# Optimization experiments

Hardware: AMD Instinct MI355X
Metric: run time of the kernel (lower is better)

The kernel has to match this reference:

```python
import jax, jax.numpy as jnp
import numpy as np
from jax import lax

B, T_IN, E, T_OUT, N_MEL = 64, 512, 512, 800, 80
P, A_LSTM, D_LSTM, ATT, NF, K = 256, 1024, 1024, 128, 32, 31
PAD = (K - 1) // 2


def setup_inputs() -> dict:
    key = jax.random.key(0)
    ks = jax.random.split(key, 24)
    s = 0.02
    d = {}
    d['encoder_outputs'] = jax.random.normal(ks[0], (B, T_IN, E), jnp.float32)
    d['decoder_inputs'] = jax.random.normal(ks[1], (B, N_MEL, T_OUT), jnp.float32)
    d['text_lengths'] = jax.random.randint(ks[2], (B,), T_IN // 2, T_IN + 1)
    # prenet (two bias-free linears)
    d['Wp1'] = jax.random.normal(ks[3], (N_MEL, P), jnp.float32) * s
    d['Wp2'] = jax.random.normal(ks[4], (P, P), jnp.float32) * s
    # attention LSTMCell: input = prenet_dim + encoder_lstm_dim
    d['Wi_a'] = jax.random.normal(ks[5], (P + E, 4 * A_LSTM), jnp.float32) * s
    d['Wh_a'] = jax.random.normal(ks[6], (A_LSTM, 4 * A_LSTM), jnp.float32) * s
    d['b_a'] = jnp.zeros((4 * A_LSTM,), jnp.float32)
    # location-sensitive attention
    d['Wq'] = jax.random.normal(ks[7], (A_LSTM, ATT), jnp.float32) * s
    d['Wm'] = jax.random.normal(ks[8], (E, ATT), jnp.float32) * s
    d['Wv'] = jax.random.normal(ks[9], (ATT,), jnp.float32) * s
    d['Kloc'] = jax.random.normal(ks[10], (NF, 2, K), jnp.float32) * s   # OIH conv kernel
    d['Wloc'] = jax.random.normal(ks[11], (NF, ATT), jnp.float32) * s
    # decoder LSTMCell: input = attention_lstm_dim + encoder_lstm_dim
    d['Wi_d'] = jax.random.normal(ks[12], (A_LSTM + E, 4 * D_LSTM), jnp.float32) * s
    d['Wh_d'] = jax.random.normal(ks[13], (D_LSTM, 4 * D_LSTM), jnp.float32) * s
    d['b_d'] = jnp.zeros((4 * D_LSTM,), jnp.float32)
    # projections from [decoder_hidden ; attention_context]
    d['Wproj'] = jax.random.normal(ks[14], (D_LSTM + E, N_MEL), jnp.float32) * s
    d['bproj'] = jnp.zeros((N_MEL,), jnp.float32)
    d['Wgate'] = jax.random.normal(ks[15], (D_LSTM + E,), jnp.float32) * s
    d['bgate'] = jnp.zeros((), jnp.float32)
    return d


def _lstm_cell(x, h, c, Wi, Wh, b):
    g = x @ Wi + h @ Wh + b
    i, f, gg, o = jnp.split(g, 4, axis=-1)  # torch LSTMCell gate order i,f,g,o
    c = jax.nn.sigmoid(f) * c + jax.nn.sigmoid(i) * jnp.tanh(gg)
    h = jax.nn.sigmoid(o) * jnp.tanh(c)
    return h, c


def reference(encoder_outputs, decoder_inputs, text_lengths,
              Wp1, Wp2, Wi_a, Wh_a, b_a, Wq, Wm, Wv, Kloc, Wloc,
              Wi_d, Wh_d, b_d, Wproj, bproj, Wgate, bgate):
    b, t_in, e = encoder_outputs.shape
    t_out = decoder_inputs.shape[2]
    valid = jnp.arange(t_in)[None, :] < text_lengths[:, None]  # [B,T_in]
    pm = encoder_outputs @ Wm                                   # processed memory [B,T_in,ATT]

    # parse_decoder_inputs + go frame -> [T_out, B, n_mel] (n_frames_per_step=1)
    x = jnp.transpose(decoder_inputs, (2, 0, 1))
    x = jnp.concatenate([jnp.zeros((1, b, N_MEL), x.dtype), x], 0)[:t_out]
    # prenet over all steps (dropout disabled: eval-mode reference)
    h = jax.nn.relu(jax.nn.relu(x @ Wp1) @ Wp2)                 # [T_out,B,P]

    def step(carry, xt):
        ah, ac, dh, dc, aw, awc, ctx = carry
        ah, ac = _lstm_cell(jnp.concatenate([xt, ctx], -1), ah, ac, Wi_a, Wh_a, b_a)
        cat = jnp.stack([aw, awc], axis=1)                      # [B,2,T_in]
        loc = lax.conv_general_dilated(cat, Kloc, (1,), [(PAD, PAD)],
                                       dimension_numbers=('NCH', 'OIH', 'NCH'))  # [B,NF,T_in]
        ploc = jnp.einsum('bft,fa->bta', loc, Wloc)             # [B,T_in,ATT]
        energies = jnp.einsum('bta,a->bt',
                              jnp.tanh((ah @ Wq)[:, None, :] + ploc + pm), Wv)
        energies = jnp.where(valid, energies, -1e9)
        aw = jax.nn.softmax(energies, axis=1)                   # [B,T_in]
        ctx = jnp.einsum('bt,bte->be', aw, encoder_outputs)
        awc = awc + aw
        dh, dc = _lstm_cell(jnp.concatenate([ah, ctx], -1), dh, dc, Wi_d, Wh_d, b_d)
        hc = jnp.concatenate([dh, ctx], -1)
        mel = hc @ Wproj + bproj                                # [B,N_MEL]
        gate = hc @ Wgate + bgate                               # [B]
        return (ah, ac, dh, dc, aw, awc, ctx), (mel, gate, aw)

    z = lambda *s: jnp.zeros(s, encoder_outputs.dtype)
    init = (z(b, A_LSTM), z(b, A_LSTM), z(b, D_LSTM), z(b, D_LSTM),
            z(b, t_in), z(b, t_in), z(b, e))
    _, (mels, gates, aws) = lax.scan(step, init, h)
    mel_outputs = jnp.transpose(mels, (1, 2, 0))                # [B,N_MEL,T_out]
    gate_outputs = jnp.transpose(gates, (1, 0))                 # [B,T_out]
    alignments = jnp.transpose(aws, (1, 0, 2))                  # [B,T_out,T_in]
    return mel_outputs, gate_outputs, alignments
```

## Files before the change

kernel.cpp:

```cpp
#include <hip/hip_runtime.h>
#include <math.h>

#define NBLK 256
#define NTHR 512

#define BB    64
#define TIN   512
#define EEE   512
#define TOUTT 800
#define NMEL  80
#define PPP   256
#define ALS   1024
#define DLS   1024
#define ATTD  128
#define KA    1792
#define KD    2560

typedef _Float16 f16;
typedef f16 f16x8 __attribute__((ext_vector_type(8)));
typedef f16 f16x2 __attribute__((ext_vector_type(2)));
typedef float f32x4 __attribute__((ext_vector_type(4)));
typedef unsigned long long u64;

#define WTA_OFF   0ull
#define WTD_OFF   3670016ull
#define PM16_OFF  8912896ull
#define ENC16_OFF 11010048ull
#define PRE_OFF   19398656ull
#define XA_OFF    25952256ull
#define XD_OFF    26066944ull
#define AH16_OFF  26230784ull
#define DH16_OFF  26263552ull
#define CTX16_OFF 26296320ull
#define EN_OFF    26329088ull
#define WQT_OFF   26361856ull
#define WPJT_OFF  26427392ull
#define WP1T_OFF  26489600ull
#define WP2T_OFF  26499840ull
#define WLP_OFF   26532608ull
#define KLP_OFF   26534656ull
#define BAR_OFF   26535648ull

#define PL_O   0
#define RED_O  512
#define QL_O   528
#define PART_O 664

__device__ __forceinline__ float sigm(float x) { return 1.0f / (1.0f + __expf(-x)); }
__device__ __forceinline__ float ftanh(float x) {
  return 1.f - 2.f / (__expf(2.f * x) + 1.f);
}

union pk32 { unsigned u; f16x2 h; float f; };
__device__ __forceinline__ unsigned packh2(float a, float b) {
  pk32 p; p.h[0] = (f16)a; p.h[1] = (f16)b; return p.u;
}

__device__ __forceinline__ u64 ld64cg(const void* p) {
  return __hip_atomic_load((const u64*)p, __ATOMIC_RELAXED, __HIP_MEMORY_SCOPE_AGENT);
}
__device__ __forceinline__ void stu16cg(void* p, unsigned short v) {
  __hip_atomic_store((unsigned short*)p, v, __ATOMIC_RELAXED, __HIP_MEMORY_SCOPE_AGENT);
}
__device__ __forceinline__ void stu32cg(void* p, unsigned v) {
  __hip_atomic_store((unsigned*)p, v, __ATOMIC_RELAXED, __HIP_MEMORY_SCOPE_AGENT);
}
__device__ __forceinline__ f16x8 ld128cg(const f16* p) {
  union { u64 q[2]; f16x8 v; } r;
  r.q[0] = ld64cg(p);
  r.q[1] = ld64cg(p + 4);
  return r.v;
}

__device__ __forceinline__ size_t fragaddr(int b, int k) {
  return (size_t)(k >> 5) * 2048 + (size_t)(b >> 4) * 512 +
         (size_t)(((b & 15) + (((k & 31) >> 3) << 4)) << 3) + (k & 7);
}

__device__ __forceinline__ void gbar(unsigned* bar, unsigned& n, bool full) {
  n += 1;
  __syncthreads();
  if (threadIdx.x == 0) {
    if (full) __threadfence();
    __hip_atomic_fetch_add(&bar[(blockIdx.x & 15) << 4], 1u, __ATOMIC_RELAXED, __HIP_MEMORY_SCOPE_AGENT);
  }
  if (threadIdx.x < 64) {
    const unsigned tgt = n * 16u;
    const unsigned g = (threadIdx.x & 15) << 4;
    asm volatile("" ::: "memory");
    while (!__all((threadIdx.x >= 16) ||
                  (__hip_atomic_load(&bar[g], __ATOMIC_RELAXED, __HIP_MEMORY_SCOPE_AGENT) >= tgt)))
      __builtin_amdgcn_s_sleep(1);
    asm volatile("" ::: "memory");
    if (full) __threadfence();
  }
  __syncthreads();
}

__global__ void __launch_bounds__(256) transA(const float* __restrict__ Wi,
                                              const float* __restrict__ Wh,
                                              f16* __restrict__ Wt) {
  __shared__ float tile[64][65];
  const int tid = threadIdx.x;
  const int kb = (int)blockIdx.x % 28;
  const int cb = (int)blockIdx.x / 28;
  const int k0 = kb * 64, c0 = cb * 64;
  for (int i = tid; i < 4096; i += 256) {
    const int r = i >> 6, c = i & 63;
    const int k = k0 + r;
    const float v = (k < 768) ? Wi[(size_t)k * 4096 + c0 + c]
                              : Wh[(size_t)(k - 768) * 4096 + c0 + c];
    tile[c][r] = v;
  }
  __syncthreads();
  for (int i = tid; i < 4096; i += 256) {
    const int c = i >> 6, kk = i & 63;
    Wt[(size_t)(c0 + c) * KA + k0 + kk] = (f16)tile[c][kk];
  }
}

__global__ void __launch_bounds__(256) transD(const float* __restrict__ Wi,
                                              const float* __restrict__ Wh,
                                              f16* __restrict__ Wt) {
  __shared__ float tile[64][65];
  const int tid = threadIdx.x;
  const int kb = (int)blockIdx.x % 40;
  const int cb = (int)blockIdx.x / 40;
  const int k0 = kb * 64, c0 = cb * 64;
  for (int i = tid; i < 4096; i += 256) {
    const int r = i >> 6, c = i & 63;
    const int k = k0 + r;
    const float v = (k < 1536) ? Wi[(size_t)k * 4096 + c0 + c]
                               : Wh[(size_t)(k - 1536) * 4096 + c0 + c];
    tile[c][r] = v;
  }
  __syncthreads();
  for (int i = tid; i < 4096; i += 256) {
    const int c = i >> 6, kk = i & 63;
    Wt[(size_t)(c0 + c) * KD + k0 + kk] = (f16)tile[c][kk];
  }
}

__global__ void __launch_bounds__(128) pmk(const float* __restrict__ enc,
                                           const float* __restrict__ Wm,
                                           f16* __restrict__ pm16) {
  __shared__ float er[512];
  const int tid = threadIdx.x;
  const int b = (int)blockIdx.x >> 9, tt = (int)blockIdx.x & 511;
  for (int i = tid; i < 512; i += 128) er[i] = enc[((size_t)b * TIN + tt) * EEE + i];
  __syncthreads();
  float s = 0.f;
  #pragma unroll 4
  for (int k = 0; k < 512; ++k) s += er[k] * Wm[k * ATTD + tid];
  pm16[((size_t)b * TIN + tt) * ATTD + tid] = (f16)s;
}

__global__ void __launch_bounds__(512) enc16k(const float* __restrict__ enc,
                                              f16* __restrict__ e16) {
  const size_t i = ((size_t)blockIdx.x * 512 + threadIdx.x) * 8;
  const float4 v0 = *reinterpret_cast<const float4*>(enc + i);
  const float4 v1 = *reinterpret_cast<const float4*>(enc + i + 4);
  f16x8 o;
  o[0] = (f16)v0.x; o[1] = (f16)v0.y; o[2] = (f16)v0.z; o[3] = (f16)v0.w;
  o[4] = (f16)v1.x; o[5] = (f16)v1.y; o[6] = (f16)v1.z; o[7] = (f16)v1.w;
  *reinterpret_cast<f16x8*>(e16 + i) = o;
}

__global__ void __launch_bounds__(256) kwk(const float* __restrict__ Kloc,
                                           const float* __restrict__ Wloc,
                                           f16* __restrict__ kwb) {
  const int idx = (int)blockIdx.x * 256 + (int)threadIdx.x;
  const int kc = idx >> 7, a = idx & 127;
  const int k = kc >> 1, cch = kc & 1;
  float s = 0.f;
  if (k < 31) {
    #pragma unroll 8
    for (int f = 0; f < 32; ++f)
      s += Kloc[f * 62 + cch * 31 + k] * Wloc[f * 128 + a];
  }
  const int ct = a >> 4, n = a & 15;
  const int ks = kc >> 5, kcl = kc & 31, kch = kcl >> 3, j = kcl & 7;
  kwb[((size_t)(ct * 2 + ks) * 64 + (kch * 16 + n)) * 8 + j] = (f16)s;
}

__global__ void __launch_bounds__(512) transAux(const float* __restrict__ Wq,
                                                const float* __restrict__ Wproj,
                                                const float* __restrict__ Wgate,
                                                const float* __restrict__ Wp1,
                                                const float* __restrict__ Wp2,
                                                f16* __restrict__ wqt,
                                                f16* __restrict__ wpjt,
                                                f16* __restrict__ wp1t,
                                                f16* __restrict__ wp2t) {
  const int idx = (int)blockIdx.x * 512 + (int)threadIdx.x;
  if (idx < 131072) {
    const int a = idx >> 10, k = idx & 1023;
    wqt[idx] = (f16)Wq[k * 128 + a];
  } else if (idx < 131072 + 124416) {
    const int j = idx - 131072;
    const int m = j / 1536, k = j % 1536;
    wpjt[j] = (f16)(m < 80 ? Wproj[k * 80 + m] : Wgate[k]);
  } else if (idx < 131072 + 124416 + 20480) {
    const int j = idx - (131072 + 124416);
    const int col = j / 80, k = j % 80;
    wp1t[j] = (f16)Wp1[k * 256 + col];
  } else if (idx < 131072 + 124416 + 20480 + 65536) {
    const int j = idx - (131072 + 124416 + 20480);
    const int col = j >> 8, k = j & 255;
    wp2t[j] = (f16)Wp2[k * 256 + col];
  }
}

__global__ void __launch_bounds__(512) prenetk(const float* __restrict__ dec_in,
                                               const f16* __restrict__ wp1t,
                                               const f16* __restrict__ wp2t,
                                               f16* __restrict__ pre) {
  __shared__ float xl[64 * 80];
  __shared__ f16 h1l[64 * 264];
  const int t = (int)blockIdx.x;
  const int tid = threadIdx.x;
  f16* out = pre + (size_t)t * 16384;
  if (t == 0) {
    unsigned* o32 = (unsigned*)out;
    for (int i = tid; i < 8192; i += 512) o32[i] = 0u;
    return;
  }
  for (int i = tid; i < 5120; i += 512) {
    const int b = i / 80, m = i % 80;
    xl[b * 80 + m] = dec_in[(size_t)b * (NMEL * TOUTT) + (size_t)m * TOUTT + (t - 1)];
  }
  __syncthreads();
  {
    const int col = tid & 255, bh = tid >> 8;
    for (int bb = 0; bb < 32; ++bb) {
      const int b = bh * 32 + bb;
      float s = 0.f;
      #pragma unroll 4
      for (int k = 0; k < 80; ++k) s += xl[b * 80 + k] * (float)wp1t[col * 80 + k];
      h1l[b * 264 + col] = (f16)fmaxf(s, 0.f);
    }
  }
  __syncthreads();
  {
    const int col = tid & 255, bh = tid >> 8;
    for (int bb = 0; bb < 32; ++bb) {
      const int b = bh * 32 + bb;
      float s = 0.f;
      #pragma unroll 4
      for (int k = 0; k < 256; ++k) s += (float)h1l[b * 264 + k] * (float)wp2t[col * 256 + k];
      out[fragaddr(b, col)] = (f16)fmaxf(s, 0.f);
    }
  }
}

__device__ __forceinline__ void lstm_tail(int bid, int tid, float* smemf,
                                          const f32x4 c, int kh, int mt, int lane,
                                          const float* __restrict__ bias, float& creg,
                                          f16* __restrict__ h16,
                                          f16* frag1, int k1off,
                                          f16* frag2, int k2off) {
  float* Call = smemf;
  float* CallB = smemf + 1024;
  const int r0 = mt * 16 + (lane >> 4) * 4;
  const int n = lane & 15;
  if (kh == 1) {
    #pragma unroll
    for (int j = 0; j < 4; ++j) CallB[(r0 + j) * 16 + n] = c[j];
  }
  __syncthreads();
  if (kh == 0) {
    #pragma unroll
    for (int j = 0; j < 4; ++j) Call[(r0 + j) * 16 + n] = c[j] + CallB[(r0 + j) * 16 + n];
  }
  __syncthreads();
  if (tid < 256) {
    const int b = tid & 63, q = tid >> 6;
    const int cc = bid * 4 + q;
    const float g0 = Call[b * 16 + q]      + bias[cc];
    const float g1 = Call[b * 16 + 4 + q]  + bias[1024 + cc];
    const float g2 = Call[b * 16 + 8 + q]  + bias[2048 + cc];
    const float g3 = Call[b * 16 + 12 + q] + bias[3072 + cc];
    const float cn = sigm(g1) * creg + sigm(g0) * ftanh(g2);
    creg = cn;
    const float h = sigm(g3) * ftanh(cn);
    pk32 hp; hp.h[0] = (f16)h; hp.h[1] = (f16)0.f;
    const unsigned short hu = (unsigned short)(hp.u & 0xFFFFu);
    stu16cg(h16 + (size_t)b * 1024 + cc, hu);
    if (frag1) stu16cg(frag1 + fragaddr(b, k1off + cc), hu);
    if (frag2) stu16cg(frag2 + fragaddr(b, k2off + cc), hu);
  }
}

__device__ __forceinline__ void do_melgate(int b, int half, int tcol,
                                           const f16* __restrict__ dh16,
                                           const f16* __restrict__ ctx16p,
                                           const f16* __restrict__ wpjt,
                                           const float* __restrict__ bproj,
                                           const float* __restrict__ bgate,
                                           float* __restrict__ out_mel,
                                           float* __restrict__ out_gate,
                                           float* smem) {
  const int tid = threadIdx.x;
  __syncthreads();
  u64* dhl = (u64*)smem;
  u64* ctl = (u64*)smem + 256;
  if (tid < 256)      dhl[tid] = ld64cg((const u64*)(dh16 + (size_t)b * 1024) + tid);
  else if (tid < 384) ctl[tid - 256] = ld64cg((const u64*)(ctx16p + (size_t)b * 512) + (tid - 256));
  __syncthreads();
  float* melp = smem + 768;
  const int nrow = half ? 40 : 41;
  const int ml = tid / 12, kq = tid % 12;
  if (ml < nrow) {
    const int m = half * 41 + ml;
    const f16* wr = wpjt + (size_t)m * 1536 + kq * 128;
    const f16* xl = (kq < 8) ? ((const f16*)dhl + kq * 128)
                             : ((const f16*)ctl + (kq - 8) * 128);
    float s = 0.f;
    #pragma unroll
    for (int c8 = 0; c8 < 16; ++c8) {
      const f16x8 xv = *reinterpret_cast<const f16x8*>(xl + c8 * 8);
      const f16x8 wv = *reinterpret_cast<const f16x8*>(wr + c8 * 8);
      #pragma unroll
      for (int j = 0; j < 8; ++j) s += (float)xv[j] * (float)wv[j];
    }
    melp[ml * 12 + kq] = s;
  }
  __syncthreads();
  if (tid < nrow) {
    float s = 0.f;
    #pragma unroll
    for (int j = 0; j < 12; ++j) s += melp[tid * 12 + j];
    const int m = half * 41 + tid;
    if (m < 80) out_mel[(size_t)b * NMEL * TOUTT + (size_t)m * TOUTT + tcol] = s + bproj[m];
    else        out_gate[(size_t)b * TOUTT + tcol] = s + bgate[0];
  }
}

__global__ void __launch_bounds__(NTHR, 1)
decoder_loop(const int* __restrict__ tlen,
             const float* __restrict__ b_a, const float* __restrict__ b_d,
             const float* __restrict__ Wv,
             const float* __restrict__ bproj, const float* __restrict__ bgate,
             const f16* __restrict__ wta_h, const f16* __restrict__ wtd_h,
             const f16* __restrict__ pm16, const f16* __restrict__ enc16,
             const f16* __restrict__ pre_h,
             const f16* __restrict__ wqt, const f16* __restrict__ wpjt,
             const f16* __restrict__ kwb,
             f16* __restrict__ xa_h, f16* __restrict__ xd_h,
             f16* __restrict__ ah16, f16* __restrict__ dh16,
             f16* __restrict__ ctx16,
             unsigned* bar,
             float* __restrict__ out_mel, float* __restrict__ out_gate,
             float* __restrict__ out_align) {
  __shared__ f16 wfA[28672];
  __shared__ f16 wfD[40960];
  __shared__ float smem[2048];
  __shared__ unsigned awb[544];

  const int tid = threadIdx.x;
  const int bid = (int)blockIdx.x;
  const int lane = tid & 63;
  const int w = tid >> 6;
  const int mt = w & 3, kh = w >> 2;
  const int b = bid & 63;
  const int chn = bid >> 6;
  unsigned syncn = 0;

  for (int i = tid; i < 3584; i += NTHR) {
    const int ks = i >> 6, l = i & 63;
    const int n = l & 15, kc = (l >> 4) * 8;
    const int gcol = (n >> 2) * 1024 + bid * 4 + (n & 3);
    const uint4 v = *reinterpret_cast<const uint4*>(wta_h + (size_t)gcol * KA + ks * 32 + kc);
    *reinterpret_cast<uint4*>(&wfA[(size_t)i * 8]) = v;
  }
  for (int i = tid; i < 5120; i += NTHR) {
    const int ks = i >> 6, l = i & 63;
    const int n = l & 15, kc = (l >> 4) * 8;
    const int gcol = (n >> 2) * 1024 + bid * 4 + (n & 3);
    const uint4 v = *reinterpret_cast<const uint4*>(wtd_h + (size_t)gcol * KD + ks * 32 + kc);
    *reinterpret_cast<uint4*>(&wfD[(size_t)i * 8]) = v;
  }
  for (int i = tid; i < 544; i += NTHR) awb[i] = 0u;
  {
    unsigned* za = (unsigned*)xa_h;
    const int gid = bid * NTHR + tid;
    for (int i = gid; i < 278528; i += NBLK * NTHR) za[i] = 0u;
  }
  gbar(bar, syncn, true);

  const int len = tlen[b];
  float awcf = 0.f;
  float cregA = 0.f, cregD = 0.f;

  for (int t = 0; t <= TOUTT; ++t) {
    if (t > 0) {
      const f16* xdP = xd_h + (size_t)((t - 1) & 1) * 163840;
      const f16* abase = xdP + (size_t)(kh * 40) * 2048 + mt * 512 + lane * 8;
      const f16* bbase = wfD + ((size_t)(kh * 40) * 64 + lane) * 8;
      f32x4 c = {0.f, 0.f, 0.f, 0.f};
      #pragma unroll 8
      for (int ks = 0; ks < 40; ++ks) {
        const f16x8 af = ld128cg(abase + (size_t)ks * 2048);
        const f16x8 bf = *reinterpret_cast<const f16x8*>(bbase + (size_t)ks * 512);
        c = __builtin_amdgcn_mfma_f32_16x16x32_f16(af, bf, c, 0, 0, 0);
      }
      lstm_tail(bid, tid, smem, c, kh, mt, lane, b_d, cregD, dh16,
                xd_h + (size_t)(t & 1) * 163840, 1536, (f16*)0, 0);
    }
    if (t < TOUTT) {
      const f16* xaP = xa_h + (size_t)(t & 1) * 114688;
      const f16* preP = pre_h + (size_t)t * 16384;
      const f16* bbase = wfA + ((size_t)(kh * 28) * 64 + lane) * 8;
      f32x4 c = {0.f, 0.f, 0.f, 0.f};
      #pragma unroll 8
      for (int ks = 0; ks < 28; ++ks) {
        const int kg = kh * 28 + ks;
        const f16* ap = (kg < 8) ? preP : xaP;
        const f16x8 af = (kg < 8)
            ? *reinterpret_cast<const f16x8*>(ap + (size_t)kg * 2048 + mt * 512 + lane * 8)
            : ld128cg(ap + (size_t)kg * 2048 + mt * 512 + lane * 8);
        const f16x8 bf = *reinterpret_cast<const f16x8*>(bbase + (size_t)ks * 512);
        c = __builtin_amdgcn_mfma_f32_16x16x32_f16(af, bf, c, 0, 0, 0);
      }
      lstm_tail(bid, tid, smem, c, kh, mt, lane, b_a, cregA, ah16,
                xa_h + (size_t)((t + 1) & 1) * 114688, 768,
                xd_h + (size_t)(t & 1) * 163840, 0);
    }
    gbar(bar, syncn, false);

    if (t == TOUTT) {
      if (chn == 1 || chn == 2)
        do_melgate(b, chn - 1, TOUTT - 1, dh16, ctx16 + (size_t)((TOUTT - 1) & 1) * 32768,
                   wpjt, bproj, bgate, out_mel, out_gate, smem);
      break;
    }

    {
      u64* ahl = (u64*)smem;
      if (tid < 256) ahl[tid] = ld64cg((const u64*)(ah16 + (size_t)b * 1024) + tid);
      __syncthreads();
      {
        const int a = tid & 127, kq = tid >> 7;
        const f16* arow = (const f16*)ahl + kq * 256;
        const f16* wr = wqt + (size_t)a * 1024 + kq * 256;
        float s = 0.f;
        #pragma unroll 8
        for (int c8 = 0; c8 < 32; ++c8) {
          const f16x8 xv = *reinterpret_cast<const f16x8*>(arow + c8 * 8);
          const f16x8 wv = *reinterpret_cast<const f16x8*>(wr + c8 * 8);
          #pragma unroll
          for (int j = 0; j < 8; ++j) s += (float)xv[j] * (float)wv[j];
        }
        smem[PART_O + kq * 128 + a] = s;
      }
      __syncthreads();
      if (tid < 128) {
        const int a = tid;
        smem[QL_O + a + (a >> 5)] = smem[PART_O + a] + smem[PART_O + 128 + a] +
                                    smem[PART_O + 256 + a] + smem[PART_O + 384 + a];
      }
      __syncthreads();

      float qlv[8], wvv[8];
      #pragma unroll
      for (int ct = 0; ct < 8; ++ct) {
        const int a = ct * 16 + (lane & 15);
        qlv[ct] = smem[QL_O + a + (a >> 5)];
        wvv[ct] = Wv[a];
      }

      for (int rt4 = 0; rt4 < 4; ++rt4) {
        const int rt = w * 4 + rt4;
        const int r_a = rt * 16 + (lane & 15);
        f32x4 c[8];
        #pragma unroll
        for (int ct = 0; ct < 8; ++ct) c[ct] = (f32x4){0.f, 0.f, 0.f, 0.f};
        #pragma unroll
        for (int ks = 0; ks < 2; ++ks) {
          const int tap = (lane >> 4) * 4 + ks * 16;
          union { unsigned u[4]; f16x8 v; } af;
          #pragma unroll
          for (int q4 = 0; q4 < 4; ++q4) af.u[q4] = awb[1 + r_a + tap + q4];
          #pragma unroll
          for (int ct = 0; ct < 8; ++ct) {
            const f16x8 bf = *reinterpret_cast<const f16x8*>(
                kwb + ((size_t)(ct * 2 + ks) * 64 + lane) * 8);
            c[ct] = __builtin_amdgcn_mfma_f32_16x16x32_f16(af.v, bf, c[ct], 0, 0, 0);
          }
        }
        float ep[4] = {0.f, 0.f, 0.f, 0.f};
        #pragma unroll
        for (int ct = 0; ct < 8; ++ct) {
          const int a = ct * 16 + (lane & 15);
          #pragma unroll
          for (int j = 0; j < 4; ++j) {
            const int r = rt * 16 + ((lane >> 4) << 2) + j;
            const float pmv = (float)pm16[(size_t)(b * TIN + r) * ATTD + a];
            ep[j] += wvv[ct] * ftanh(qlv[ct] + c[ct][j] + pmv);
          }
        }
        #pragma unroll
        for (int j = 0; j < 4; ++j) {
          ep[j] += __shfl_xor(ep[j], 1);
          ep[j] += __shfl_xor(ep[j], 2);
          ep[j] += __shfl_xor(ep[j], 4);
          ep[j] += __shfl_xor(ep[j], 8);
        }
        if ((lane & 15) == 0) {
          #pragma unroll
          for (int j = 0; j < 4; ++j)
            smem[PL_O + rt * 16 + ((lane >> 4) << 2) + j] = ep[j];
        }
      }

      const float ee = (tid < len) ? smem[PL_O + tid] : -1e30f;
      float m = ee;
      #pragma unroll
      for (int o = 32; o > 0; o >>= 1) m = fmaxf(m, __shfl_xor(m, o));
      if (lane == 0) smem[RED_O + w] = m;
      __syncthreads();
      if (tid == 0) {
        float mm = smem[RED_O];
        #pragma unroll
        for (int i = 1; i < 8; ++i) mm = fmaxf(mm, smem[RED_O + i]);
        smem[RED_O + 8] = mm;
      }
      __syncthreads();
      const float M = smem[RED_O + 8];
      const float p = (tid < len) ? __expf(ee - M) : 0.f;
      float s = p;
      #pragma unroll
      for (int o = 32; o > 0; o >>= 1) s += __shfl_xor(s, o);
      if (lane == 0) smem[RED_O + w] = s;
      __syncthreads();
      if (tid == 0) {
        float ss = smem[RED_O];
        #pragma unroll
        for (int i = 1; i < 8; ++i) ss += smem[RED_O + i];
        smem[RED_O + 8] = ss;
      }
      __syncthreads();
      const float an = p * (1.f / smem[RED_O + 8]);
      smem[PL_O + tid] = an;
      awcf += an;
      awb[16 + tid] = packh2(an, awcf);
      if (chn == 0) out_align[((size_t)b * TOUTT + t) * TIN + tid] = an;
      __syncthreads();

      {
        const int eo = lane & 15, sub4 = lane >> 4;
        float a8[8];
        #pragma unroll
        for (int i = 0; i < 8; ++i) a8[i] = 0.f;
        const f16* ebase = enc16 + (size_t)(b * TIN) * EEE + chn * 128 + eo * 8;
        #pragma unroll 4
        for (int j = 0; j < 16; ++j) {
          const int tj = w * 64 + sub4 * 16 + j;
          const float wv = smem[PL_O + tj];
          const f16x8 ev = __builtin_nontemporal_load(
              reinterpret_cast<const f16x8*>(ebase + (size_t)tj * EEE));
          #pragma unroll
          for (int i = 0; i < 8; ++i) a8[i] += wv * (float)ev[i];
        }
        #pragma unroll
        for (int i = 0; i < 8; ++i) {
          a8[i] += __shfl_xor(a8[i], 16);
          a8[i] += __shfl_xor(a8[i], 32);
        }
        if (lane < 16) {
          #pragma unroll
          for (int i = 0; i < 8; ++i) smem[PART_O + w * 128 + eo * 8 + i] = a8[i];
        }
      }
      __syncthreads();
      if (tid < 128) {
        float v = 0.f;
        #pragma unroll
        for (int ww = 0; ww < 8; ++ww) v += smem[PART_O + ww * 128 + tid];
        smem[PL_O + tid] = v;
      }
      __syncthreads();
      if (tid < 64) {
        const int ecol = chn * 128 + 2 * tid;
        const unsigned pv = packh2(smem[PL_O + 2 * tid], smem[PL_O + 2 * tid + 1]);
        stu32cg((unsigned*)(xa_h + (size_t)((t + 1) & 1) * 114688 + fragaddr(b, 256 + ecol)), pv);
        stu32cg((unsigned*)(xd_h + (size_t)(t & 1) * 163840 + fragaddr(b, 1024 + ecol)), pv);
        stu32cg((unsigned*)(ctx16 + (size_t)(t & 1) * 32768 + (size_t)b * 512 + ecol), pv);
      }
      if (t > 0 && (chn == 1 || chn == 2))
        do_melgate(b, chn - 1, t - 1, dh16, ctx16 + (size_t)((t - 1) & 1) * 32768,
                   wpjt, bproj, bgate, out_mel, out_gate, smem);
    }
    gbar(bar, syncn, false);
  }
}

extern "C" void kernel_launch(void* const* d_in, const int* in_sizes, int n_in,
                              void* d_out, int out_size, void* d_ws, size_t ws_size,
                              hipStream_t stream) {
  (void)in_sizes; (void)n_in; (void)out_size; (void)ws_size;
  const float* enc    = (const float*)d_in[0];
  const float* dec_in = (const float*)d_in[1];
  const int*   tlen   = (const int*)d_in[2];
  const float* Wp1    = (const float*)d_in[3];
  const float* Wp2    = (const float*)d_in[4];
  const float* Wi_a   = (const float*)d_in[5];
  const float* Wh_a   = (const float*)d_in[6];
  const float* b_a    = (const float*)d_in[7];
  const float* Wq     = (const float*)d_in[8];
  const float* Wm     = (const float*)d_in[9];
  const float* Wv     = (const float*)d_in[10];
  const float* Kloc   = (const float*)d_in[11];
  const float* Wloc   = (const float*)d_in[12];
  const float* Wi_d   = (const float*)d_in[13];
  const float* Wh_d   = (const float*)d_in[14];
  const float* b_d    = (const float*)d_in[15];
  const float* Wproj  = (const float*)d_in[16];
  const float* bproj  = (const float*)d_in[17];
  const float* Wgate  = (const float*)d_in[18];
  const float* bgate  = (const float*)d_in[19];

  float* ws = (float*)d_ws;
  f16*   wta_h = (f16*)(ws + WTA_OFF);
  f16*   wtd_h = (f16*)(ws + WTD_OFF);
  f16*   pm16  = (f16*)(ws + PM16_OFF);
  f16*   e16   = (f16*)(ws + ENC16_OFF);
  f16*   pre_h = (f16*)(ws + PRE_OFF);
  f16*   xa_h  = (f16*)(ws + XA_OFF);
  f16*   xd_h  = (f16*)(ws + XD_OFF);
  f16*   ah16  = (f16*)(ws + AH16_OFF);
  f16*   dh16  = (f16*)(ws + DH16_OFF);
  f16*   ctx16 = (f16*)(ws + CTX16_OFF);
  f16*   kwb   = (f16*)(ws + EN_OFF);
  f16*   wqt   = (f16*)(ws + WQT_OFF);
  f16*   wpjt  = (f16*)(ws + WPJT_OFF);
  f16*   wp1t  = (f16*)(ws + WP1T_OFF);
  f16*   wp2t  = (f16*)(ws + WP2T_OFF);
  unsigned* bar = (unsigned*)(ws + BAR_OFF);

  float* out_mel   = (float*)d_out;
  float* out_gate  = out_mel + (size_t)BB * NMEL * TOUTT;
  float* out_align = out_gate + (size_t)BB * TOUTT;

  hipMemsetAsync(bar, 0, 272 * sizeof(unsigned), stream);
  transA<<<dim3(28 * 64), dim3(256), 0, stream>>>(Wi_a, Wh_a, wta_h);
  transD<<<dim3(40 * 64), dim3(256), 0, stream>>>(Wi_d, Wh_d, wtd_h);
  pmk<<<dim3(BB * TIN), dim3(128), 0, stream>>>(enc, Wm, pm16);
  enc16k<<<dim3(4096), dim3(512), 0, stream>>>(enc, e16);
  kwk<<<dim3(32), dim3(256), 0, stream>>>(Kloc, Wloc, kwb);
  transAux<<<dim3(667), dim3(512), 0, stream>>>(Wq, Wproj, Wgate, Wp1, Wp2,
                                                wqt, wpjt, wp1t, wp2t);
  prenetk<<<dim3(TOUTT), dim3(512), 0, stream>>>(dec_in, wp1t, wp2t, pre_h);
  decoder_loop<<<dim3(NBLK), dim3(NTHR), 0, stream>>>(
      tlen, b_a, b_d, Wv, bproj, bgate,
      wta_h, wtd_h, pm16, e16, pre_h, wqt, wpjt, kwb,
      xa_h, xd_h, ah16, dh16, ctx16, bar,
      out_mel, out_gate, out_align);
}
```

Before: 62.01 ms.

## Precompute LSTM gate partial sums before barrier to shorten critical path

Moves the K-chunks of the attention and decoder LSTM matmuls whose inputs are already available (prenet, context, the hidden state written in the previous phase) into the other phase of the step, ahead of the global barrier. After each barrier only the chunks that depend on freshly produced data remain. The loop is restructured with a peeled epilogue for the last decoder step. Output stores to mel, gate and alignment use nontemporal stores. This adds an extra __syncthreads in lstm_tail and carries accumulator registers across phases.

```diff
diff --git a/kernel.cpp b/kernel.cpp
--- a/kernel.cpp
+++ b/kernel.cpp
@@ -37,8 +37,6 @@
 #define WPJT_OFF  26427392ull
 #define WP1T_OFF  26489600ull
 #define WP2T_OFF  26499840ull
-#define WLP_OFF   26532608ull
-#define KLP_OFF   26534656ull
 #define BAR_OFF   26535648ull
 
 #define PL_O   0
@@ -70,6 +68,10 @@
   r.q[0] = ld64cg(p);
   r.q[1] = ld64cg(p + 4);
   return r.v;
+}
+__device__ __forceinline__ void stnt_f32(float* p, float v) {
+  asm volatile("global_store_dword %0, %1, off sc0 sc1 nt"
+               :: "v"(p), "v"(v) : "memory");
 }
 
 __device__ __forceinline__ size_t fragaddr(int b, int k) {
@@ -289,6 +291,7 @@
     if (frag1) stu16cg(frag1 + fragaddr(b, k1off + cc), hu);
     if (frag2) stu16cg(frag2 + fragaddr(b, k2off + cc), hu);
   }
+  __syncthreads();
 }
 
 __device__ __forceinline__ void do_melgate(int b, int half, int tcol,
@@ -331,8 +334,8 @@
     #pragma unroll
     for (int j = 0; j < 12; ++j) s += melp[tid * 12 + j];
     const int m = half * 41 + tid;
-    if (m < 80) out_mel[(size_t)b * NMEL * TOUTT + (size_t)m * TOUTT + tcol] = s + bproj[m];
-    else        out_gate[(size_t)b * TOUTT + tcol] = s + bgate[0];
+    if (m < 80) stnt_f32(out_mel + (size_t)b * NMEL * TOUTT + (size_t)m * TOUTT + tcol, s + bproj[m]);
+    else        stnt_f32(out_gate + (size_t)b * TOUTT + tcol, s + bgate[0]);
   }
 }
 
@@ -391,48 +394,77 @@
   const int len = tlen[b];
   float awcf = 0.f;
   float cregA = 0.f, cregD = 0.f;
-
-  for (int t = 0; t <= TOUTT; ++t) {
+  f32x4 cA = {0.f, 0.f, 0.f, 0.f};
+  f32x4 cD = {0.f, 0.f, 0.f, 0.f};
+
+  const f16* bbaseA = wfA + ((size_t)(kh * 28) * 64 + lane) * 8;
+  const f16* bbaseD = wfD + ((size_t)(kh * 40) * 64 + lane) * 8;
+  const int laneoff = mt * 512 + lane * 8;
+
+  for (int t = 0; t < TOUTT; ++t) {
     if (t > 0) {
-      const f16* xdP = xd_h + (size_t)((t - 1) & 1) * 163840;
-      const f16* abase = xdP + (size_t)(kh * 40) * 2048 + mt * 512 + lane * 8;
-      const f16* bbase = wfD + ((size_t)(kh * 40) * 64 + lane) * 8;
-      f32x4 c = {0.f, 0.f, 0.f, 0.f};
+      const f16* abase = xd_h + (size_t)((t - 1) & 1) * 163840 + (size_t)(kh * 40) * 2048 + laneoff;
+      const int ks0 = kh ? 0 : 32, ks1 = kh ? 8 : 40;
       #pragma unroll 8
-      for (int ks = 0; ks < 40; ++ks) {
+      for (int ks = ks0; ks < ks1; ++ks) {
         const f16x8 af = ld128cg(abase + (size_t)ks * 2048);
-        const f16x8 bf = *reinterpret_cast<const f16x8*>(bbase + (size_t)ks * 512);
-        c = __builtin_amdgcn_mfma_f32_16x16x32_f16(af, bf, c, 0, 0, 0);
-      }
-      lstm_tail(bid, tid, smem, c, kh, mt, lane, b_d, cregD, dh16,
+        const f16x8 bf = *reinterpret_cast<const f16x8*>(bbaseD + (size_t)ks * 512);
+        cD = __builtin_amdgcn_mfma_f32_16x16x32_f16(af, bf, cD, 0, 0, 0);
+      }
+    }
+    if (kh == 0) {
+      const f16* abase = xa_h + (size_t)(t & 1) * 114688 + laneoff;
+      #pragma unroll 8
+      for (int ks = 8; ks < 24; ++ks) {
+        const f16x8 af = ld128cg(abase + (size_t)ks * 2048);
+        const f16x8 bf = *reinterpret_cast<const f16x8*>(bbaseA + (size_t)ks * 512);
+        cA = __builtin_amdgcn_mfma_f32_16x16x32_f16(af, bf, cA, 0, 0, 0);
+      }
+    }
+    if (t > 0)
+      lstm_tail(bid, tid, smem, cD, kh, mt, lane, b_d, cregD, dh16,
                 xd_h + (size_t)(t & 1) * 163840, 1536, (f16*)0, 0);
-    }
-    if (t < TOUTT) {
-      const f16* xaP = xa_h + (size_t)(t & 1) * 114688;
-      const f16* preP = pre_h + (size_t)t * 16384;
-      const f16* bbase = wfA + ((size_t)(kh * 28) * 64 + lane) * 8;
-      f32x4 c = {0.f, 0.f, 0.f, 0.f};
+    lstm_tail(bid, tid, smem, cA, kh, mt, lane, b_a, cregA, ah16,
+              xa_h + (size_t)((t + 1) & 1) * 114688, 768,
+              xd_h + (size_t)(t & 1) * 163840, 0);
+    gbar(bar, syncn, false);
+
+    {
+      const f16* abase = xd_h + (size_t)(t & 1) * 163840 + (size_t)(kh * 40) * 2048 + laneoff;
+      cD = (f32x4){0.f, 0.f, 0.f, 0.f};
+      const int ks0 = kh ? 8 : 0, ks1 = kh ? 40 : 32;
       #pragma unroll 8
-      for (int ks = 0; ks < 28; ++ks) {
-        const int kg = kh * 28 + ks;
-        const f16* ap = (kg < 8) ? preP : xaP;
-        const f16x8 af = (kg < 8)
-            ? *reinterpret_cast<const f16x8*>(ap + (size_t)kg * 2048 + mt * 512 + lane * 8)
-            : ld128cg(ap + (size_t)kg * 2048 + mt * 512 + lane * 8);
-        const f16x8 bf = *reinterpret_cast<const f16x8*>(bbase + (size_t)ks * 512);
-        c = __builtin_amdgcn_mfma_f32_16x16x32_f16(af, bf, c, 0, 0, 0);
-      }
-      lstm_tail(bid, tid, smem, c, kh, mt, lane, b_a, cregA, ah16,
-                xa_h + (size_t)((t + 1) & 1) * 114688, 768,
-                xd_h + (size_t)(t & 1) * 163840, 0);
-    }
-    gbar(bar, syncn, false);
-
-    if (t == TOUTT) {
-      if (chn == 1 || chn == 2)
-        do_melgate(b, chn - 1, TOUTT - 1, dh16, ctx16 + (size_t)((TOUTT - 1) & 1) * 32768,
-                   wpjt, bproj, bgate, out_mel, out_gate, smem);
-      break;
+      for (int ks = ks0; ks < ks1; ++ks) {
+        const f16x8 af = ld128cg(abase + (size_t)ks * 2048);
+        const f16x8 bf = *reinterpret_cast<const f16x8*>(bbaseD + (size_t)ks * 512);
+        cD = __builtin_amdgcn_mfma_f32_16x16x32_f16(af, bf, cD, 0, 0, 0);
+      }
+    }
+    cA = (f32x4){0.f, 0.f, 0.f, 0.f};
+    if (t + 1 < TOUTT) {
+      const f16* xaP = xa_h + (size_t)((t + 1) & 1) * 114688;
+      const f16* preP = pre_h + (size_t)(t + 1) * 16384;
+      if (kh == 0) {
+        #pragma unroll
+        for (int ks = 0; ks < 8; ++ks) {
+          const f16x8 af = *reinterpret_cast<const f16x8*>(preP + (size_t)ks * 2048 + laneoff);
+          const f16x8 bf = *reinterpret_cast<const f16x8*>(bbaseA + (size_t)ks * 512);
+          cA = __builtin_amdgcn_mfma_f32_16x16x32_f16(af, bf, cA, 0, 0, 0);
+        }
+        #pragma unroll
+        for (int ks = 24; ks < 28; ++ks) {
+          const f16x8 af = ld128cg(xaP + (size_t)ks * 2048 + laneoff);
+          const f16x8 bf = *reinterpret_cast<const f16x8*>(bbaseA + (size_t)ks * 512);
+          cA = __builtin_amdgcn_mfma_f32_16x16x32_f16(af, bf, cA, 0, 0, 0);
+        }
+      } else {
+        #pragma unroll 8
+        for (int ks = 0; ks < 28; ++ks) {
+          const f16x8 af = ld128cg(xaP + (size_t)(28 + ks) * 2048 + laneoff);
+          const f16x8 bf = *reinterpret_cast<const f16x8*>(bbaseA + (size_t)ks * 512);
+          cA = __builtin_amdgcn_mfma_f32_16x16x32_f16(af, bf, cA, 0, 0, 0);
+        }
+      }
     }
 
     {
@@ -544,7 +576,7 @@
       smem[PL_O + tid] = an;
       awcf += an;
       awb[16 + tid] = packh2(an, awcf);
-      if (chn == 0) out_align[((size_t)b * TOUTT + t) * TIN + tid] = an;
+      if (chn == 0) stnt_f32(out_align + ((size_t)b * TOUTT + t) * TIN + tid, an);
       __syncthreads();
 
       {
@@ -592,6 +624,23 @@
                    wpjt, bproj, bgate, out_mel, out_gate, smem);
     }
     gbar(bar, syncn, false);
+  }
+
+  {
+    const f16* abase = xd_h + (size_t)((TOUTT - 1) & 1) * 163840 + (size_t)(kh * 40) * 2048 + laneoff;
+    const int ks0 = kh ? 0 : 32, ks1 = kh ? 8 : 40;
+    #pragma unroll 8
+    for (int ks = ks0; ks < ks1; ++ks) {
+      const f16x8 af = ld128cg(abase + (size_t)ks * 2048);
+      const f16x8 bf = *reinterpret_cast<const f16x8*>(bbaseD + (size_t)ks * 512);
+      cD = __builtin_amdgcn_mfma_f32_16x16x32_f16(af, bf, cD, 0, 0, 0);
+    }
+    lstm_tail(bid, tid, smem, cD, kh, mt, lane, b_d, cregD, dh16,
+              xd_h + (size_t)(TOUTT & 1) * 163840, 1536, (f16*)0, 0);
+    gbar(bar, syncn, false);
+    if (chn == 1 || chn == 2)
+      do_melgate(b, chn - 1, TOUTT - 1, dh16, ctx16 + (size_t)((TOUTT - 1) & 1) * 32768,
+                 wpjt, bproj, bgate, out_mel, out_gate, smem);
   }
 }
 
```

Result: slower. 73.77 ms (+19.0%).
